# Kernel optimization log

Hardware: AMD Instinct MI355X
Metric: run time of the kernel (lower is better)

Reference implementation:

```python
import jax, jax.numpy as jnp
import numpy as np
from jax import lax

B, T, IN, H, OUT, TGT = 8192, 100, 16, 128, 2, 60


def _cell(x, h, c, W_ih, W_hh, b_ih, b_hh):
    # torch LSTM gate order: i, f, g, o
    g = x @ W_ih.T + h @ W_hh.T + b_ih + b_hh
    i, f, gg, o = jnp.split(g, 4, axis=-1)
    i = jax.nn.sigmoid(i); f = jax.nn.sigmoid(f); o = jax.nn.sigmoid(o)
    c = f * c + i * jnp.tanh(gg)
    h = o * jnp.tanh(c)
    return h, c


def _run_layer(xs, W_ih, W_hh, b_ih, b_hh):
    # xs: [T, B, in] time-major; zero init states (torch default)
    h0 = jnp.zeros((xs.shape[1], W_hh.shape[1]), xs.dtype)
    c0 = jnp.zeros_like(h0)
    def step(carry, x_t):
        h, c = carry
        h, c = _cell(x_t, h, c, W_ih, W_hh, b_ih, b_hh)
        return (h, c), h
    (h, c), hs = lax.scan(step, (h0, c0), xs)
    return hs, h, c


def setup_inputs() -> dict:
    key = jax.random.key(0)
    ks = iter(jax.random.split(key, 24))
    s = 0.05
    d = {"x": jax.random.normal(next(ks), (B, T, IN), jnp.float32),
         "target_len": TGT}
    # encoder params (layer0 in=IN, layer1 in=H)
    d["eW_ih0"] = jax.random.normal(next(ks), (4 * H, IN)) * s
    d["eW_hh0"] = jax.random.normal(next(ks), (4 * H, H)) * s
    d["eb_ih0"] = jax.random.normal(next(ks), (4 * H,)) * s
    d["eb_hh0"] = jax.random.normal(next(ks), (4 * H,)) * s
    d["eW_ih1"] = jax.random.normal(next(ks), (4 * H, H)) * s
    d["eW_hh1"] = jax.random.normal(next(ks), (4 * H, H)) * s
    d["eb_ih1"] = jax.random.normal(next(ks), (4 * H,)) * s
    d["eb_hh1"] = jax.random.normal(next(ks), (4 * H,)) * s
    # decoder params (layer0 in=OUT, layer1 in=H)
    d["dW_ih0"] = jax.random.normal(next(ks), (4 * H, OUT)) * s
    d["dW_hh0"] = jax.random.normal(next(ks), (4 * H, H)) * s
    d["db_ih0"] = jax.random.normal(next(ks), (4 * H,)) * s
    d["db_hh0"] = jax.random.normal(next(ks), (4 * H,)) * s
    d["dW_ih1"] = jax.random.normal(next(ks), (4 * H, H)) * s
    d["dW_hh1"] = jax.random.normal(next(ks), (4 * H, H)) * s
    d["db_ih1"] = jax.random.normal(next(ks), (4 * H,)) * s
    d["db_hh1"] = jax.random.normal(next(ks), (4 * H,)) * s
    d["fcW"] = jax.random.normal(next(ks), (OUT, H)) * s
    d["fcb"] = jax.random.normal(next(ks), (OUT,)) * s
    return d


def reference(x, target_len,
              eW_ih0, eW_hh0, eb_ih0, eb_hh0, eW_ih1, eW_hh1, eb_ih1, eb_hh1,
              dW_ih0, dW_hh0, db_ih0, db_hh0, dW_ih1, dW_hh1, db_ih1, db_hh1,
              fcW, fcb):
    xs = jnp.swapaxes(x, 0, 1)  # [T, B, IN]
    hs0, h0, c0 = _run_layer(xs, eW_ih0, eW_hh0, eb_ih0, eb_hh0)
    _, h1, c1 = _run_layer(hs0, eW_ih1, eW_hh1, eb_ih1, eb_hh1)
    dec_in = x[:, -1, :2]  # [B, 2]
    def dec_step(carry, _):
        dh0, dc0, dh1, dc1, inp = carry
        dh0, dc0 = _cell(inp, dh0, dc0, dW_ih0, dW_hh0, db_ih0, db_hh0)
        dh1, dc1 = _cell(dh0, dh1, dc1, dW_ih1, dW_hh1, db_ih1, db_hh1)
        out = dh1 @ fcW.T + fcb  # [B, 2]
        return (dh0, dc0, dh1, dc1, out), out
    _, outs = lax.scan(dec_step, (h0, c0, h1, c1, dec_in), None,
                       length=int(target_len))
    return jnp.swapaxes(outs, 0, 1)  # [B, target_len, 2]
```

## Files before the change

### kernel.cpp

```cpp
#include <hip/hip_runtime.h>


using s16x8 = __attribute__((ext_vector_type(8))) short;
using h16x8 = __attribute__((ext_vector_type(8))) _Float16;
using f32x4 = __attribute__((ext_vector_type(4))) float;

#define DEV static __device__ __forceinline__

DEV unsigned short f2h(float f) {
  _Float16 h = (_Float16)f;
  return __builtin_bit_cast(unsigned short, h);
}
DEV float h2f(short h) {
  return (float)__builtin_bit_cast(_Float16, (unsigned short)h);
}
DEV float rcp_(float x) { return __builtin_amdgcn_rcpf(x); }
DEV float sigm(float v) { return rcp_(1.0f + __expf(-v)); }
DEV float tanh_(float v) {
  float e = __expf(-2.0f * fabsf(v));
  float r = (1.0f - e) * rcp_(1.0f + e);
  return v < 0.0f ? -r : r;
}
DEV f32x4 mf(s16x8 a, s16x8 b, f32x4 c) {
  return __builtin_amdgcn_mfma_f32_16x16x32_f16(
      __builtin_bit_cast(h16x8, a), __builtin_bit_cast(h16x8, b), c, 0, 0, 0);
}
DEV f32x4 splat4(float v) { f32x4 r = {v, v, v, v}; return r; }

DEV int swz(int row, int slot) { return row * 256 + (((slot ^ row) & 15) << 4); }
DEV s16x8 ldA(const char* buf, int rt, int ks, int lo, int hi) {
  return *(const s16x8*)(buf + swz(rt * 16 + lo, ks * 4 + hi));
}
DEV s16x8 ldB(const char* wlds, int colbase, int ks, int lo, int hi) {
  return *(const s16x8*)(wlds + swz(colbase + lo, ks * 4 + hi));
}
DEV void storeH(char* buf, int row, int col, unsigned short v) {
  int addr = row * 256 + ((((col >> 3) ^ row) & 15) << 4) + (col & 7) * 2;
  *(unsigned short*)(buf + addr) = v;
}
DEV unsigned short cellup(float gi, float gf, float gg, float go, float& c) {
  float i = sigm(gi), f = sigm(gf), g2 = tanh_(gg), o = sigm(go);
  c = f * c + i * g2;
  return f2h(o * tanh_(c));
}

#define WS_WX  917504
#define WS_IME 950272
#define WS_IMD 1048576

__global__ void prep_kernel(
    const float* __restrict__ eWih0, const float* __restrict__ eWhh0,
    const float* __restrict__ eWih1, const float* __restrict__ eWhh1,
    const float* __restrict__ dWih0, const float* __restrict__ dWhh0,
    const float* __restrict__ dWih1, const float* __restrict__ dWhh1,
    const float* __restrict__ fcW, char* __restrict__ ws) {
  int idx = blockIdx.x * 256 + threadIdx.x;
  if (idx < 57344) {
    int m = idx >> 13, r = idx & 8191;
    int col = r >> 4, ks = (r >> 2) & 3, hi = r & 3;
    s16x8 v;
    if (m == 6) {
      float w0 = dWih0[col * 2 + 0], w1 = dWih0[col * 2 + 1];
#pragma unroll
      for (int j = 0; j < 8; ++j) {
        int k = ks * 32 + hi * 8 + j;
        v[j] = (short)f2h(w0 * fcW[k] + w1 * fcW[128 + k]);
      }
    } else {
      const float* W;
      switch (m) {
        case 0: W = eWih1; break;
        case 1: W = eWhh1; break;
        case 2: W = dWih1; break;
        case 3: W = dWhh1; break;
        case 4: W = eWhh0; break;
        default: W = dWhh0; break;
      }
      const float* p = W + col * 128 + ks * 32 + hi * 8;
#pragma unroll
      for (int j = 0; j < 8; ++j) v[j] = (short)f2h(p[j]);
    }
    *(s16x8*)(ws + m * 131072 + ks * 32768 + col * 64 + hi * 16) = v;
  } else if (idx < 59392) {
    int r3 = idx - 57344;
    int col = r3 >> 2, hi = r3 & 3;
    s16x8 v;
#pragma unroll
    for (int j = 0; j < 8; ++j) v[j] = 0;
    if (hi < 2) {
      const float* p = eWih0 + col * 16 + hi * 8;
#pragma unroll
      for (int j = 0; j < 8; ++j) v[j] = (short)f2h(p[j]);
    }
    *(s16x8*)(ws + WS_WX + col * 64 + hi * 16) = v;
  } else if (idx < 71680) {
    int r2 = idx - 59392;
    int m = (r2 >= 6144), rr = m ? r2 - 6144 : r2;
    int row = rr >> 4, s = rr & 15;
    const float* p = (m ? dWhh0 : eWhh0) + row * 128 + s * 8;
    s16x8 v;
#pragma unroll
    for (int j = 0; j < 8; ++j) v[j] = (short)f2h(p[j]);
    *(s16x8*)(ws + (m ? WS_IMD : WS_IME) + row * 256 + (((s ^ row) & 15) << 4)) = v;
  }
}

#define SMEM_BYTES 136960

__global__ __launch_bounds__(512, 2) void fused_kernel(
    const float* __restrict__ x,
    const float* __restrict__ ebih0, const float* __restrict__ ebhh0,
    const float* __restrict__ ebih1, const float* __restrict__ ebhh1,
    const float* __restrict__ dWih0,
    const float* __restrict__ dbih0, const float* __restrict__ dbhh0,
    const float* __restrict__ dbih1, const float* __restrict__ dbhh1,
    const float* __restrict__ fcW, const float* __restrict__ fcb,
    const char* __restrict__ ws, float* __restrict__ out) {
  extern __shared__ char smem[];
  char* wL   = smem;
  char* h0B  = smem + 98304;
  char* h1B  = smem + 114688;
  char* xB   = smem + 131072;
  float* inpL = (float*)(smem + 136192);
  char* fcwL = smem + 136448;

  const int tid = threadIdx.x;
  const int w = tid >> 6, l = tid & 63, lo = l & 15, hi = l >> 4;
  const int row0 = blockIdx.x * 32;
  const int colb = w * 16;
  const int obase = (colb + lo) * 64 + hi * 16;
  const int obase3 = obase + 384 * 64;

  {
    const int4* src = (const int4*)(ws + WS_IME);
    int4* dst = (int4*)wL;
    for (int i = tid; i < 6144; i += 512) dst[i] = src[i];
  }
  {
    int4 z = make_int4(0, 0, 0, 0);
    int4* p = (int4*)h0B;
    for (int i = tid; i < 2368; i += 512) p[i] = z;
  }

  float b0[4], b1[4];
  s16x8 wx0[4];
#pragma unroll
  for (int g = 0; g < 4; ++g) {
    int col = g * 128 + colb + lo;
    b0[g] = ebih0[col] + ebhh0[col];
    b1[g] = ebih1[col] + ebhh1[col];
    wx0[g] = *(const s16x8*)(ws + WS_WX + g * 8192 + obase);
  }
  float c0s[2][4], c1s[2][4];
#pragma unroll
  for (int rt = 0; rt < 2; ++rt)
#pragma unroll
    for (int r = 0; r < 4; ++r) { c0s[rt][r] = 0.f; c1s[rt][r] = 0.f; }

  const int xr = tid >> 4, xf = tid & 15;
  const float* xrow = x + (long long)(row0 + xr) * 1600 + xf;
  *(unsigned short*)(xB + xr * 80 + xf * 2) = f2h(xrow[0]);
  float xv = xrow[16];
  int cur = 0;
  __syncthreads();

  for (int k = 0; k <= 100; ++k) {
    char* h0r = h0B + cur * 8192;
    char* h0w = h0B + (cur ^ 1) * 8192;
    char* h1r = h1B + cur * 8192;
    char* h1w = h1B + (cur ^ 1) * 8192;
    char* xc  = xB + cur * 2560;
    char* xn  = xB + (cur ^ 1) * 2560;

    float xv_stage = xv;
    if (k < 98) xv = xrow[(k + 2) * 16];

    if (k > 0) {
      f32x4 acc[2][4];
#pragma unroll
      for (int g = 0; g < 4; ++g) { acc[0][g] = splat4(b1[g]); acc[1][g] = splat4(b1[g]); }
      int lf = 0;
      asm("" : "+s"(lf));
      const char* W1 = ws + lf;
#pragma unroll
      for (int s = 0; s < 8; ++s) {
        const char* src = (s < 4) ? h0r : h1r;
        int ks = s & 3;
        const char* wk = W1 + (s < 4 ? 0 : 131072) + ks * 32768 + obase;
        s16x8 a0 = ldA(src, 0, ks, lo, hi), a1 = ldA(src, 1, ks, lo, hi);
#pragma unroll
        for (int g = 0; g < 4; ++g) {
          s16x8 bb = *(const s16x8*)(wk + g * 8192);
          acc[0][g] = mf(a0, bb, acc[0][g]);
          acc[1][g] = mf(a1, bb, acc[1][g]);
        }
      }
#pragma unroll
      for (int rt = 0; rt < 2; ++rt)
#pragma unroll
        for (int r = 0; r < 4; ++r)
          storeH(h1w, rt * 16 + hi * 4 + r, colb + lo,
                 cellup(acc[rt][0][r], acc[rt][1][r], acc[rt][2][r], acc[rt][3][r], c1s[rt][r]));
    }

    __builtin_amdgcn_sched_barrier(0x30);

    if (k < 100) {
      f32x4 acc[2][4];
#pragma unroll
      for (int g = 0; g < 4; ++g) { acc[0][g] = splat4(b0[g]); acc[1][g] = splat4(b0[g]); }
      {
        s16x8 a0 = *(const s16x8*)(xc + lo * 80 + hi * 16);
        s16x8 a1 = *(const s16x8*)(xc + (16 + lo) * 80 + hi * 16);
#pragma unroll
        for (int g = 0; g < 4; ++g) {
          acc[0][g] = mf(a0, wx0[g], acc[0][g]);
          acc[1][g] = mf(a1, wx0[g], acc[1][g]);
        }
      }
      int lf = 0;
      asm("" : "+s"(lf));
      const char* W0 = ws + 4 * 131072 + lf;
#pragma unroll
      for (int ks = 0; ks < 4; ++ks) {
        s16x8 a0 = ldA(h0r, 0, ks, lo, hi), a1 = ldA(h0r, 1, ks, lo, hi);
#pragma unroll
        for (int g = 0; g < 3; ++g) {
          s16x8 bb = ldB(wL, g * 128 + colb, ks, lo, hi);
          acc[0][g] = mf(a0, bb, acc[0][g]);
          acc[1][g] = mf(a1, bb, acc[1][g]);
        }
        s16x8 b3 = *(const s16x8*)(W0 + ks * 32768 + obase3);
        acc[0][3] = mf(a0, b3, acc[0][3]);
        acc[1][3] = mf(a1, b3, acc[1][3]);
      }
#pragma unroll
      for (int rt = 0; rt < 2; ++rt)
#pragma unroll
        for (int r = 0; r < 4; ++r)
          storeH(h0w, rt * 16 + hi * 4 + r, colb + lo,
                 cellup(acc[rt][0][r], acc[rt][1][r], acc[rt][2][r], acc[rt][3][r], c0s[rt][r]));
      if (k < 99)
        *(unsigned short*)(xn + xr * 80 + xf * 2) = f2h(xv_stage);
    }
    __syncthreads();
    cur ^= 1;
  }
  int dc0 = cur ^ 1, dc1 = cur;

  {
    const int4* src = (const int4*)(ws + WS_IMD);
    int4* dst = (int4*)wL;
    for (int i = tid; i < 6144; i += 512) dst[i] = src[i];
  }
  if (tid < 64) {
    int r = tid >> 1, o = tid & 1;
    inpL[r * 2 + o] = x[(long long)(row0 + r) * 1600 + 1584 + o];
  }
  if (tid < 256) {
    int o = tid >> 7, k2 = tid & 127;
    *(unsigned short*)(fcwL + o * 256 + k2 * 2) = f2h(fcW[o * 128 + k2]);
  }
  float dwx[4][2], b0f[4];
#pragma unroll
  for (int g = 0; g < 4; ++g) {
    int col = g * 128 + colb + lo;
    b0[g] = dbih0[col] + dbhh0[col];
    b1[g] = dbih1[col] + dbhh1[col];
    dwx[g][0] = dWih0[col * 2 + 0];
    dwx[g][1] = dWih0[col * 2 + 1];
  }
  float fb0 = fcb[0], fb1 = fcb[1];
#pragma unroll
  for (int g = 0; g < 4; ++g) b0f[g] = b0[g] + dwx[g][0] * fb0 + dwx[g][1] * fb1;
  __syncthreads();

  {
    f32x4 acc[2][4];
    char* h0r = h0B + dc0 * 8192;
    char* h0w = h0B + (dc0 ^ 1) * 8192;
#pragma unroll
    for (int rt = 0; rt < 2; ++rt)
#pragma unroll
      for (int r = 0; r < 4; ++r) {
        float2 ip = *(const float2*)(inpL + (rt * 16 + hi * 4 + r) * 2);
#pragma unroll
        for (int g = 0; g < 4; ++g)
          acc[rt][g][r] = b0[g] + ip.x * dwx[g][0] + ip.y * dwx[g][1];
      }
    int lf = 0;
    asm("" : "+s"(lf));
    const char* WA = ws + 5 * 131072 + lf;
#pragma unroll
    for (int ks = 0; ks < 4; ++ks) {
      s16x8 a0 = ldA(h0r, 0, ks, lo, hi), a1 = ldA(h0r, 1, ks, lo, hi);
#pragma unroll
      for (int g = 0; g < 3; ++g) {
        s16x8 bb = ldB(wL, g * 128 + colb, ks, lo, hi);
        acc[0][g] = mf(a0, bb, acc[0][g]);
        acc[1][g] = mf(a1, bb, acc[1][g]);
      }
      s16x8 b3 = *(const s16x8*)(WA + ks * 32768 + obase3);
      acc[0][3] = mf(a0, b3, acc[0][3]);
      acc[1][3] = mf(a1, b3, acc[1][3]);
    }
#pragma unroll
    for (int rt = 0; rt < 2; ++rt)
#pragma unroll
      for (int r = 0; r < 4; ++r)
        storeH(h0w, rt * 16 + hi * 4 + r, colb + lo,
               cellup(acc[rt][0][r], acc[rt][1][r], acc[rt][2][r], acc[rt][3][r], c0s[rt][r]));
    dc0 ^= 1;
    __syncthreads();
  }

  for (int t = 0; t < 60; ++t) {
    {
      char* h0r = h0B + dc0 * 8192;
      char* h1r = h1B + dc1 * 8192;
      char* h1w = h1B + (dc1 ^ 1) * 8192;
      f32x4 acc[2][4];
#pragma unroll
      for (int g = 0; g < 4; ++g) { acc[0][g] = splat4(b1[g]); acc[1][g] = splat4(b1[g]); }
      int lf = 0;
      asm("" : "+s"(lf));
      const char* WB = ws + 2 * 131072 + lf;
#pragma unroll
      for (int s = 0; s < 8; ++s) {
        const char* src = (s < 4) ? h0r : h1r;
        int ks = s & 3;
        const char* wk = WB + (s < 4 ? 0 : 131072) + ks * 32768 + obase;
        s16x8 a0 = ldA(src, 0, ks, lo, hi), a1 = ldA(src, 1, ks, lo, hi);
#pragma unroll
        for (int g = 0; g < 4; ++g) {
          s16x8 bb = *(const s16x8*)(wk + g * 8192);
          acc[0][g] = mf(a0, bb, acc[0][g]);
          acc[1][g] = mf(a1, bb, acc[1][g]);
        }
      }
#pragma unroll
      for (int rt = 0; rt < 2; ++rt)
#pragma unroll
        for (int r = 0; r < 4; ++r)
          storeH(h1w, rt * 16 + hi * 4 + r, colb + lo,
                 cellup(acc[rt][0][r], acc[rt][1][r], acc[rt][2][r], acc[rt][3][r], c1s[rt][r]));
      dc1 ^= 1;
      __syncthreads();
    }

    {
      char* h1r = h1B + dc1 * 8192;
      if (w < 2) {
        int row = w * 16 + lo;
        int o = hi & 1, kh = hi >> 1;
        float sum = 0.f;
#pragma unroll
        for (int cc = 0; cc < 8; ++cc) {
          s16x8 hv = *(const s16x8*)(h1r + swz(row, kh * 8 + cc));
          s16x8 wv = *(const s16x8*)(fcwL + o * 256 + (kh * 8 + cc) * 16);
#pragma unroll
          for (int j = 0; j < 8; ++j) sum += h2f(hv[j]) * h2f(wv[j]);
        }
        sum += __shfl_xor(sum, 32, 64);
        if (l < 32)
          out[((long long)(row0 + row) * 60 + t) * 2 + o] = sum + (o ? fb1 : fb0);
      }
      if (t < 59) {
        char* h0r = h0B + dc0 * 8192;
        char* h0w = h0B + (dc0 ^ 1) * 8192;
        f32x4 acc[2][4];
#pragma unroll
        for (int g = 0; g < 4; ++g) { acc[0][g] = splat4(b0f[g]); acc[1][g] = splat4(b0f[g]); }
        int lf = 0;
        asm("" : "+s"(lf));
        const char* WA = ws + 5 * 131072 + lf;
        const char* WC = ws + 6 * 131072 + lf;
#pragma unroll
        for (int ks = 0; ks < 4; ++ks) {
          s16x8 a0 = ldA(h0r, 0, ks, lo, hi), a1 = ldA(h0r, 1, ks, lo, hi);
          s16x8 e0 = ldA(h1r, 0, ks, lo, hi), e1 = ldA(h1r, 1, ks, lo, hi);
#pragma unroll
          for (int g = 0; g < 3; ++g) {
            s16x8 bb = ldB(wL, g * 128 + colb, ks, lo, hi);
            acc[0][g] = mf(a0, bb, acc[0][g]);
            acc[1][g] = mf(a1, bb, acc[1][g]);
          }
          s16x8 b3 = *(const s16x8*)(WA + ks * 32768 + obase3);
          acc[0][3] = mf(a0, b3, acc[0][3]);
          acc[1][3] = mf(a1, b3, acc[1][3]);
#pragma unroll
          for (int g = 0; g < 4; ++g) {
            s16x8 bc = *(const s16x8*)(WC + ks * 32768 + g * 8192 + obase);
            acc[0][g] = mf(e0, bc, acc[0][g]);
            acc[1][g] = mf(e1, bc, acc[1][g]);
          }
        }
#pragma unroll
        for (int rt = 0; rt < 2; ++rt)
#pragma unroll
          for (int r = 0; r < 4; ++r)
            storeH(h0w, rt * 16 + hi * 4 + r, colb + lo,
                   cellup(acc[rt][0][r], acc[rt][1][r], acc[rt][2][r], acc[rt][3][r], c0s[rt][r]));
        dc0 ^= 1;
      }
      __syncthreads();
    }
  }
}

extern "C" void kernel_launch(void* const* d_in, const int* in_sizes, int n_in,
                              void* d_out, int out_size, void* d_ws, size_t ws_size,
                              hipStream_t stream) {
  (void)in_sizes; (void)n_in; (void)out_size; (void)ws_size;
  const float* x      = (const float*)d_in[0];
  const float* eWih0  = (const float*)d_in[2];
  const float* eWhh0  = (const float*)d_in[3];
  const float* ebih0  = (const float*)d_in[4];
  const float* ebhh0  = (const float*)d_in[5];
  const float* eWih1  = (const float*)d_in[6];
  const float* eWhh1  = (const float*)d_in[7];
  const float* ebih1  = (const float*)d_in[8];
  const float* ebhh1  = (const float*)d_in[9];
  const float* dWih0  = (const float*)d_in[10];
  const float* dWhh0  = (const float*)d_in[11];
  const float* dbih0  = (const float*)d_in[12];
  const float* dbhh0  = (const float*)d_in[13];
  const float* dWih1  = (const float*)d_in[14];
  const float* dWhh1  = (const float*)d_in[15];
  const float* dbih1  = (const float*)d_in[16];
  const float* dbhh1  = (const float*)d_in[17];
  const float* fcW    = (const float*)d_in[18];
  const float* fcb    = (const float*)d_in[19];
  float* out          = (float*)d_out;
  char* ws            = (char*)d_ws;

  prep_kernel<<<280, 256, 0, stream>>>(eWih0, eWhh0, eWih1, eWhh1,
                                       dWih0, dWhh0, dWih1, dWhh1, fcW, ws);

  hipFuncSetAttribute(reinterpret_cast<const void*>(fused_kernel),
                      hipFuncAttributeMaxDynamicSharedMemorySize, SMEM_BYTES);

  fused_kernel<<<256, 512, SMEM_BYTES, stream>>>(
      x, ebih0, ebhh0, ebih1, ebhh1, dWih0, dbih0, dbhh0, dbih1, dbhh1,
      fcW, fcb, ws, out);
}
```

Measured before the change: 1.186 ms.

## Software-pipeline global weight loads, simplify tanh, and parallelize FC output across waves

Weight fragments streamed from global memory are now prefetched one k-step ahead into double-buffered registers (bf0/bf1, cf0/cf1), and the gate-3 fragments are hoisted out of the k loop, so load latency overlaps with the MFMA work. The tanh drops the abs/sign branch in favour of the form 1-2/(exp(2v)+1). The FC output reduction is spread over all eight waves with shuffle reductions instead of using two waves. Shared memory moves from dynamic to a static array, and the sched_barrier is removed. The prefetch buffers raise VGPR pressure under the two-blocks-per-CU launch bound, and the new tanh can overflow exp for large inputs, though rcp of inf should still yield ±1.

Result: faster. 1.153 ms (-2.8%).

```diff
diff --git a/kernel.cpp b/kernel.cpp
--- a/kernel.cpp
+++ b/kernel.cpp
@@ -17,9 +17,8 @@
 DEV float rcp_(float x) { return __builtin_amdgcn_rcpf(x); }
 DEV float sigm(float v) { return rcp_(1.0f + __expf(-v)); }
 DEV float tanh_(float v) {
-  float e = __expf(-2.0f * fabsf(v));
-  float r = (1.0f - e) * rcp_(1.0f + e);
-  return v < 0.0f ? -r : r;
+  float e = __expf(2.0f * v);
+  return 1.0f - 2.0f * rcp_(e + 1.0f);
 }
 DEV f32x4 mf(s16x8 a, s16x8 b, f32x4 c) {
   return __builtin_amdgcn_mfma_f32_16x16x32_f16(
@@ -105,8 +104,6 @@
   }
 }
 
-#define SMEM_BYTES 136960
-
 __global__ __launch_bounds__(512, 2) void fused_kernel(
     const float* __restrict__ x,
     const float* __restrict__ ebih0, const float* __restrict__ ebhh0,
@@ -116,7 +113,7 @@
     const float* __restrict__ dbih1, const float* __restrict__ dbhh1,
     const float* __restrict__ fcW, const float* __restrict__ fcb,
     const char* __restrict__ ws, float* __restrict__ out) {
-  extern __shared__ char smem[];
+  __shared__ __align__(16) char smem[136960];
   char* wL   = smem;
   char* h0B  = smem + 98304;
   char* h1B  = smem + 114688;
@@ -182,17 +179,26 @@
       int lf = 0;
       asm("" : "+s"(lf));
       const char* W1 = ws + lf;
+      s16x8 bf0[4], bf1[4];
+#pragma unroll
+      for (int g = 0; g < 4; ++g)
+        bf0[g] = *(const s16x8*)(W1 + g * 8192 + obase);
 #pragma unroll
       for (int s = 0; s < 8; ++s) {
+        s16x8* bcur = (s & 1) ? bf1 : bf0;
+        s16x8* bnxt = (s & 1) ? bf0 : bf1;
+        if (s < 7) {
+          const char* wkn = W1 + ((s + 1) < 4 ? 0 : 131072) + ((s + 1) & 3) * 32768 + obase;
+#pragma unroll
+          for (int g = 0; g < 4; ++g) bnxt[g] = *(const s16x8*)(wkn + g * 8192);
+        }
         const char* src = (s < 4) ? h0r : h1r;
         int ks = s & 3;
-        const char* wk = W1 + (s < 4 ? 0 : 131072) + ks * 32768 + obase;
         s16x8 a0 = ldA(src, 0, ks, lo, hi), a1 = ldA(src, 1, ks, lo, hi);
 #pragma unroll
         for (int g = 0; g < 4; ++g) {
-          s16x8 bb = *(const s16x8*)(wk + g * 8192);
-          acc[0][g] = mf(a0, bb, acc[0][g]);
-          acc[1][g] = mf(a1, bb, acc[1][g]);
+          acc[0][g] = mf(a0, bcur[g], acc[0][g]);
+          acc[1][g] = mf(a1, bcur[g], acc[1][g]);
         }
       }
 #pragma unroll
@@ -203,12 +209,17 @@
                  cellup(acc[rt][0][r], acc[rt][1][r], acc[rt][2][r], acc[rt][3][r], c1s[rt][r]));
     }
 
-    __builtin_amdgcn_sched_barrier(0x30);
-
     if (k < 100) {
       f32x4 acc[2][4];
 #pragma unroll
       for (int g = 0; g < 4; ++g) { acc[0][g] = splat4(b0[g]); acc[1][g] = splat4(b0[g]); }
+      int lf = 0;
+      asm("" : "+s"(lf));
+      const char* W0 = ws + 4 * 131072 + lf;
+      s16x8 b3[4];
+#pragma unroll
+      for (int ks = 0; ks < 4; ++ks)
+        b3[ks] = *(const s16x8*)(W0 + ks * 32768 + obase3);
       {
         s16x8 a0 = *(const s16x8*)(xc + lo * 80 + hi * 16);
         s16x8 a1 = *(const s16x8*)(xc + (16 + lo) * 80 + hi * 16);
@@ -218,9 +229,6 @@
           acc[1][g] = mf(a1, wx0[g], acc[1][g]);
         }
       }
-      int lf = 0;
-      asm("" : "+s"(lf));
-      const char* W0 = ws + 4 * 131072 + lf;
 #pragma unroll
       for (int ks = 0; ks < 4; ++ks) {
         s16x8 a0 = ldA(h0r, 0, ks, lo, hi), a1 = ldA(h0r, 1, ks, lo, hi);
@@ -230,9 +238,8 @@
           acc[0][g] = mf(a0, bb, acc[0][g]);
           acc[1][g] = mf(a1, bb, acc[1][g]);
         }
-        s16x8 b3 = *(const s16x8*)(W0 + ks * 32768 + obase3);
-        acc[0][3] = mf(a0, b3, acc[0][3]);
-        acc[1][3] = mf(a1, b3, acc[1][3]);
+        acc[0][3] = mf(a0, b3[ks], acc[0][3]);
+        acc[1][3] = mf(a1, b3[ks], acc[1][3]);
       }
 #pragma unroll
       for (int rt = 0; rt < 2; ++rt)
@@ -291,6 +298,10 @@
     int lf = 0;
     asm("" : "+s"(lf));
     const char* WA = ws + 5 * 131072 + lf;
+    s16x8 b3[4];
+#pragma unroll
+    for (int ks = 0; ks < 4; ++ks)
+      b3[ks] = *(const s16x8*)(WA + ks * 32768 + obase3);
 #pragma unroll
     for (int ks = 0; ks < 4; ++ks) {
       s16x8 a0 = ldA(h0r, 0, ks, lo, hi), a1 = ldA(h0r, 1, ks, lo, hi);
@@ -300,9 +311,8 @@
         acc[0][g] = mf(a0, bb, acc[0][g]);
         acc[1][g] = mf(a1, bb, acc[1][g]);
       }
-      s16x8 b3 = *(const s16x8*)(WA + ks * 32768 + obase3);
-      acc[0][3] = mf(a0, b3, acc[0][3]);
-      acc[1][3] = mf(a1, b3, acc[1][3]);
+      acc[0][3] = mf(a0, b3[ks], acc[0][3]);
+      acc[1][3] = mf(a1, b3[ks], acc[1][3]);
     }
 #pragma unroll
     for (int rt = 0; rt < 2; ++rt)
@@ -325,17 +335,26 @@
       int lf = 0;
       asm("" : "+s"(lf));
       const char* WB = ws + 2 * 131072 + lf;
+      s16x8 bf0[4], bf1[4];
+#pragma unroll
+      for (int g = 0; g < 4; ++g)
+        bf0[g] = *(const s16x8*)(WB + g * 8192 + obase);
 #pragma unroll
       for (int s = 0; s < 8; ++s) {
+        s16x8* bcur = (s & 1) ? bf1 : bf0;
+        s16x8* bnxt = (s & 1) ? bf0 : bf1;
+        if (s < 7) {
+          const char* wkn = WB + ((s + 1) < 4 ? 0 : 131072) + ((s + 1) & 3) * 32768 + obase;
+#pragma unroll
+          for (int g = 0; g < 4; ++g) bnxt[g] = *(const s16x8*)(wkn + g * 8192);
+        }
         const char* src = (s < 4) ? h0r : h1r;
         int ks = s & 3;
-        const char* wk = WB + (s < 4 ? 0 : 131072) + ks * 32768 + obase;
         s16x8 a0 = ldA(src, 0, ks, lo, hi), a1 = ldA(src, 1, ks, lo, hi);
 #pragma unroll
         for (int g = 0; g < 4; ++g) {
-          s16x8 bb = *(const s16x8*)(wk + g * 8192);
-          acc[0][g] = mf(a0, bb, acc[0][g]);
-          acc[1][g] = mf(a1, bb, acc[1][g]);
+          acc[0][g] = mf(a0, bcur[g], acc[0][g]);
+          acc[1][g] = mf(a1, bcur[g], acc[1][g]);
         }
       }
 #pragma unroll
@@ -350,20 +369,22 @@
 
     {
       char* h1r = h1B + dc1 * 8192;
-      if (w < 2) {
-        int row = w * 16 + lo;
-        int o = hi & 1, kh = hi >> 1;
+      {
+        int rl = l >> 4, oo = (l >> 3) & 1, seg = l & 7;
+        int row = w * 4 + rl;
+        s16x8 hv0 = *(const s16x8*)(h1r + swz(row, seg));
+        s16x8 wv0 = *(const s16x8*)(fcwL + oo * 256 + seg * 16);
+        s16x8 hv1 = *(const s16x8*)(h1r + swz(row, seg + 8));
+        s16x8 wv1 = *(const s16x8*)(fcwL + oo * 256 + (seg + 8) * 16);
         float sum = 0.f;
 #pragma unroll
-        for (int cc = 0; cc < 8; ++cc) {
-          s16x8 hv = *(const s16x8*)(h1r + swz(row, kh * 8 + cc));
-          s16x8 wv = *(const s16x8*)(fcwL + o * 256 + (kh * 8 + cc) * 16);
-#pragma unroll
-          for (int j = 0; j < 8; ++j) sum += h2f(hv[j]) * h2f(wv[j]);
-        }
-        sum += __shfl_xor(sum, 32, 64);
-        if (l < 32)
-          out[((long long)(row0 + row) * 60 + t) * 2 + o] = sum + (o ? fb1 : fb0);
+        for (int j = 0; j < 8; ++j)
+          sum += h2f(hv0[j]) * h2f(wv0[j]) + h2f(hv1[j]) * h2f(wv1[j]);
+        sum += __shfl_xor(sum, 1);
+        sum += __shfl_xor(sum, 2);
+        sum += __shfl_xor(sum, 4);
+        if (seg == 0)
+          out[((long long)(row0 + row) * 60 + t) * 2 + oo] = sum + (oo ? fb1 : fb0);
       }
       if (t < 59) {
         char* h0r = h0B + dc0 * 8192;
@@ -375,8 +396,23 @@
         asm("" : "+s"(lf));
         const char* WA = ws + 5 * 131072 + lf;
         const char* WC = ws + 6 * 131072 + lf;
+        s16x8 b3[4];
+#pragma unroll
+        for (int ks = 0; ks < 4; ++ks)
+          b3[ks] = *(const s16x8*)(WA + ks * 32768 + obase3);
+        s16x8 cf0[4], cf1[4];
+#pragma unroll
+        for (int g = 0; g < 4; ++g)
+          cf0[g] = *(const s16x8*)(WC + g * 8192 + obase);
 #pragma unroll
         for (int ks = 0; ks < 4; ++ks) {
+          s16x8* ccur = (ks & 1) ? cf1 : cf0;
+          s16x8* cnxt = (ks & 1) ? cf0 : cf1;
+          if (ks < 3) {
+            const char* wkn = WC + (ks + 1) * 32768 + obase;
+#pragma unroll
+            for (int g = 0; g < 4; ++g) cnxt[g] = *(const s16x8*)(wkn + g * 8192);
+          }
           s16x8 a0 = ldA(h0r, 0, ks, lo, hi), a1 = ldA(h0r, 1, ks, lo, hi);
           s16x8 e0 = ldA(h1r, 0, ks, lo, hi), e1 = ldA(h1r, 1, ks, lo, hi);
 #pragma unroll
@@ -385,14 +421,12 @@
             acc[0][g] = mf(a0, bb, acc[0][g]);
             acc[1][g] = mf(a1, bb, acc[1][g]);
           }
-          s16x8 b3 = *(const s16x8*)(WA + ks * 32768 + obase3);
-          acc[0][3] = mf(a0, b3, acc[0][3]);
-          acc[1][3] = mf(a1, b3, acc[1][3]);
+          acc[0][3] = mf(a0, b3[ks], acc[0][3]);
+          acc[1][3] = mf(a1, b3[ks], acc[1][3]);
 #pragma unroll
           for (int g = 0; g < 4; ++g) {
-            s16x8 bc = *(const s16x8*)(WC + ks * 32768 + g * 8192 + obase);
-            acc[0][g] = mf(e0, bc, acc[0][g]);
-            acc[1][g] = mf(e1, bc, acc[1][g]);
+            acc[0][g] = mf(e0, ccur[g], acc[0][g]);
+            acc[1][g] = mf(e1, ccur[g], acc[1][g]);
           }
         }
 #pragma unroll
@@ -437,10 +471,7 @@
   prep_kernel<<<280, 256, 0, stream>>>(eWih0, eWhh0, eWih1, eWhh1,
                                        dWih0, dWhh0, dWih1, dWhh1, fcW, ws);
 
-  hipFuncSetAttribute(reinterpret_cast<const void*>(fused_kernel),
-                      hipFuncAttributeMaxDynamicSharedMemorySize, SMEM_BYTES);
-
-  fused_kernel<<<256, 512, SMEM_BYTES, stream>>>(
+  fused_kernel<<<256, 512, 0, stream>>>(
       x, ebih0, ebhh0, ebih1, ebhh1, dWih0, dbih0, dbhh0, dbih1, dbhh1,
       fcW, fcb, ws, out);
 }
```
